# Optimization experiments

Hardware: AMD Instinct MI355X
Metric: run time of the kernel (lower is better)

## Reference

```python
import jax, jax.numpy as jnp
import numpy as np

B, S, D, H, DH, SD = 4, 512, 768, 12, 64, 30
ALPHA, BETA = 1.0, 1.0


def setup_inputs() -> dict:
    root = jax.random.key(0)
    ks = jax.random.split(root, 16)
    n = lambda k, sh: jax.random.normal(k, sh, dtype=jnp.float32)
    w = lambda k, sh: 0.02 * jax.random.normal(k, sh, dtype=jnp.float32)
    return {
        "key": n(ks[0], (B, S, D)),
        "value": n(ks[1], (B, S, D)),
        "query": n(ks[2], (B, S, D)),
        "structure": n(ks[3], (B, S, S, SD)),
        "mask": jax.random.randint(ks[4], (B, S, S), 0, 2).astype(bool),
        "Wq": w(ks[5], (D, D)), "bq": jnp.zeros((D,), jnp.float32),
        "Wk": w(ks[6], (D, D)), "bk": jnp.zeros((D,), jnp.float32),
        "Wv": w(ks[7], (D, D)), "bv": jnp.zeros((D,), jnp.float32),
        "Wsk": w(ks[8], (SD, DH)), "bsk": jnp.zeros((DH,), jnp.float32),
        "Wsv": w(ks[9], (SD, DH)), "bsv": jnp.zeros((DH,), jnp.float32),
        "Wo": w(ks[10], (D, D)), "bo": jnp.zeros((D,), jnp.float32),
    }


def reference(key, value, query, structure, mask,
              Wq, bq, Wk, bk, Wv, bv, Wsk, bsk, Wsv, bsv, Wo, bo):
    # shape: [B,S,D] -> [B,H,S,DH]
    def proj(x, W, b):
        return (x @ W + b).reshape(B, -1, H, DH).transpose(0, 2, 1, 3)

    q = proj(query, Wq, bq) / np.float32(np.sqrt(DH))  # scale applied before both score terms
    k = proj(key, Wk, bk)
    v = proj(value, Wv, bv)

    sk = structure @ Wsk + bsk  # [B,Q,K,DH] relative-structure keys
    sv = structure @ Wsv + bsv  # [B,Q,K,DH] relative-structure values

    scores = jnp.einsum('bhqd,bhkd->bhqk', q, k)
    scores = scores + ALPHA * jnp.einsum('bhqd,bqkd->bhqk', q, sk)
    scores = jnp.where(mask[:, None, :, :], jnp.float32(-1e18), scores)

    attn = jax.nn.softmax(scores, axis=-1)  # dropout p=0 -> identity

    ctx = jnp.einsum('bhqk,bhkd->bhqd', attn, v)
    ctx = ctx + BETA * jnp.einsum('bhqk,bqkd->bhqd', attn, sv)
    ctx = ctx.transpose(0, 2, 1, 3).reshape(B, S, D)

    output = ctx @ Wo + bo
    top_attn = attn[:, 0]  # [B,Q,K]
    return output, top_attn
```

## Files before the change

### kernel.cpp

```cpp
#include <hip/hip_runtime.h>
#include <hip/hip_bf16.h>

typedef unsigned int uint32_ty;

typedef float  nfloat2 __attribute__((ext_vector_type(2)));
typedef float  nfloat4 __attribute__((ext_vector_type(4)));
typedef int    nint4   __attribute__((ext_vector_type(4)));
typedef short  bf16x8  __attribute__((ext_vector_type(8)));
typedef float  f32x4   __attribute__((ext_vector_type(4)));
typedef unsigned short ushort4n __attribute__((ext_vector_type(4)));

#define BB 4
#define SS 512
#define DD 768
#define HH 12
#define DHH 64
#define SDD 30

#define LP 520

__device__ __forceinline__ float bfu(unsigned short u) {
    return __uint_as_float(((uint32_ty)u) << 16);
}
__device__ __forceinline__ unsigned short tobf(float f) {
    return __bfloat16_as_ushort(__float2bfloat16(f));
}
__device__ __forceinline__ uint32_ty pk2(float a, float b) {
    return ((uint32_ty)tobf(a)) | ((uint32_ty)tobf(b) << 16);
}
__device__ __forceinline__ void unp8(uint4 u, float* t) {
    t[0] = __uint_as_float(u.x << 16);
    t[1] = __uint_as_float(u.x & 0xFFFF0000u);
    t[2] = __uint_as_float(u.y << 16);
    t[3] = __uint_as_float(u.y & 0xFFFF0000u);
    t[4] = __uint_as_float(u.z << 16);
    t[5] = __uint_as_float(u.z & 0xFFFF0000u);
    t[6] = __uint_as_float(u.w << 16);
    t[7] = __uint_as_float(u.w & 0xFFFF0000u);
}
__device__ __forceinline__ void unp4(uint2 u, float* t) {
    t[0] = __uint_as_float(u.x << 16);
    t[1] = __uint_as_float(u.x & 0xFFFF0000u);
    t[2] = __uint_as_float(u.y << 16);
    t[3] = __uint_as_float(u.y & 0xFFFF0000u);
}

__global__ __launch_bounds__(256) void cvt_x(
    const float* __restrict__ k_in, const float* __restrict__ v_in,
    unsigned short* __restrict__ kb, unsigned short* __restrict__ vb)
{
    const float* in = blockIdx.z ? v_in : k_in;
    unsigned short* out = blockIdx.z ? vb : kb;
    size_t i = (size_t)blockIdx.x * 256 + threadIdx.x;
    const float4* p = (const float4*)in;
    float4 a = p[2 * i], b = p[2 * i + 1];
    uint4 pk;
    pk.x = pk2(a.x, a.y); pk.y = pk2(a.z, a.w);
    pk.z = pk2(b.x, b.y); pk.w = pk2(b.z, b.w);
    ((uint4*)out)[i] = pk;
}

__global__ __launch_bounds__(256) void cvt_wT(
    const float* __restrict__ W0, const float* __restrict__ W1,
    const float* __restrict__ W2, const float* __restrict__ W3,
    unsigned short* __restrict__ T0, unsigned short* __restrict__ T1,
    unsigned short* __restrict__ T2, unsigned short* __restrict__ T3)
{
    __shared__ float tile[64][65];
    int z = blockIdx.z;
    const float* W = (z == 0) ? W0 : (z == 1) ? W1 : (z == 2) ? W2 : W3;
    unsigned short* T = (z == 0) ? T0 : (z == 1) ? T1 : (z == 2) ? T2 : T3;
    int k0 = blockIdx.y * 64, n0 = blockIdx.x * 64;
    int tid = threadIdx.x;
#pragma unroll
    for (int rep = 0; rep < 4; rep++) {
        int i = tid + 256 * rep;
        int r = i >> 4, c4 = i & 15;
        float4 wv = *(const float4*)(W + (size_t)(k0 + r) * DD + n0 + 4 * c4);
        tile[r][4 * c4 + 0] = wv.x; tile[r][4 * c4 + 1] = wv.y;
        tile[r][4 * c4 + 2] = wv.z; tile[r][4 * c4 + 3] = wv.w;
    }
    __syncthreads();
#pragma unroll
    for (int rep = 0; rep < 2; rep++) {
        int i = tid + 256 * rep;
        int n = i >> 3, kc = i & 7;
        uint4 pk;
        pk.x = pk2(tile[8 * kc + 0][n], tile[8 * kc + 1][n]);
        pk.y = pk2(tile[8 * kc + 2][n], tile[8 * kc + 3][n]);
        pk.z = pk2(tile[8 * kc + 4][n], tile[8 * kc + 5][n]);
        pk.w = pk2(tile[8 * kc + 6][n], tile[8 * kc + 7][n]);
        *(uint4*)(T + (size_t)(n0 + n) * DD + k0 + 8 * kc) = pk;
    }
}

#define MBM 64
#define MBN 64
#define MBK 64
#define LDK 72

__global__ __launch_bounds__(256) void gemm_proj3(
    const float* __restrict__ Xq,
    const unsigned short* __restrict__ Xkb, const unsigned short* __restrict__ Xvb,
    const unsigned short* __restrict__ WTq, const unsigned short* __restrict__ WTk,
    const unsigned short* __restrict__ WTv,
    const float* __restrict__ bq, const float* __restrict__ bk, const float* __restrict__ bv,
    float* __restrict__ oq, unsigned short* __restrict__ okT, unsigned short* __restrict__ ov)
{
    __shared__ unsigned short As[MBM][LDK];
    __shared__ unsigned short Bs[MBN][LDK];
    int z = blockIdx.z;
    const unsigned short* WT = (z == 0) ? WTq : (z == 1) ? WTk : WTv;
    const float* bias = (z == 0) ? bq : (z == 1) ? bk : bv;

    int tid = threadIdx.x;
    int lane = tid & 63, wave = tid >> 6;
    int m0 = blockIdx.y * MBM, n0 = blockIdx.x * MBN;
    int wm = (wave >> 1) * 32, wn = (wave & 1) * 32;
    int fr = lane & 15, fq = lane >> 4;

    f32x4 acc[2][2];
#pragma unroll
    for (int i = 0; i < 2; i++)
#pragma unroll
        for (int j = 0; j < 2; j++) acc[i][j] = (f32x4){0.f, 0.f, 0.f, 0.f};

    for (int k0 = 0; k0 < DD; k0 += MBK) {
        if (z == 0) {
#pragma unroll
            for (int rep = 0; rep < 4; rep++) {
                int i = tid + 256 * rep;
                int r = i >> 4, c4 = i & 15;
                float4 xv = *(const float4*)(Xq + (size_t)(m0 + r) * DD + k0 + 4 * c4);
                ushort4n pk = {tobf(xv.x), tobf(xv.y), tobf(xv.z), tobf(xv.w)};
                *(ushort4n*)&As[r][4 * c4] = pk;
            }
        } else {
            const unsigned short* Xb = (z == 1) ? Xkb : Xvb;
#pragma unroll
            for (int rep = 0; rep < 2; rep++) {
                int i = tid + 256 * rep;
                int r = i >> 3, c = i & 7;
                *(uint4*)&As[r][8 * c] =
                    *(const uint4*)(Xb + (size_t)(m0 + r) * DD + k0 + 8 * c);
            }
        }
#pragma unroll
        for (int rep = 0; rep < 2; rep++) {
            int i = tid + 256 * rep;
            int r = i >> 3, c = i & 7;
            *(uint4*)&Bs[r][8 * c] =
                *(const uint4*)(WT + (size_t)(n0 + r) * DD + k0 + 8 * c);
        }
        __syncthreads();
#pragma unroll
        for (int ks = 0; ks < 2; ks++) {
            bf16x8 a0 = *(bf16x8*)&As[wm + fr][ks * 32 + fq * 8];
            bf16x8 a1 = *(bf16x8*)&As[wm + 16 + fr][ks * 32 + fq * 8];
            bf16x8 b0 = *(bf16x8*)&Bs[wn + fr][ks * 32 + fq * 8];
            bf16x8 b1 = *(bf16x8*)&Bs[wn + 16 + fr][ks * 32 + fq * 8];
            acc[0][0] = __builtin_amdgcn_mfma_f32_16x16x32_bf16(a0, b0, acc[0][0], 0, 0, 0);
            acc[0][1] = __builtin_amdgcn_mfma_f32_16x16x32_bf16(a0, b1, acc[0][1], 0, 0, 0);
            acc[1][0] = __builtin_amdgcn_mfma_f32_16x16x32_bf16(a1, b0, acc[1][0], 0, 0, 0);
            acc[1][1] = __builtin_amdgcn_mfma_f32_16x16x32_bf16(a1, b1, acc[1][1], 0, 0, 0);
        }
        __syncthreads();
    }

#pragma unroll
    for (int i = 0; i < 2; i++) {
#pragma unroll
        for (int j = 0; j < 2; j++) {
            int n = n0 + wn + 16 * j + fr;
            int h = n >> 6, d = n & 63;
            float bn = bias[n];
            int mbase = m0 + wm + 16 * i + fq * 4;
            int b = mbase >> 9, sbase = mbase & 511;
            if (z == 1) {
                ushort4n pk;
#pragma unroll
                for (int r = 0; r < 4; r++) pk[r] = tobf(acc[i][j][r] + bn);
                *(ushort4n*)(okT + ((((size_t)b * HH + h) * DHH + d) * SS + sbase)) = pk;
            } else if (z == 0) {
#pragma unroll
                for (int r = 0; r < 4; r++)
                    oq[((((size_t)b * HH + h) * SS + sbase + r) * DHH + d)] =
                        (acc[i][j][r] + bn) * 0.125f;
            } else {
#pragma unroll
                for (int r = 0; r < 4; r++)
                    ov[((((size_t)b * HH + h) * SS + sbase + r) * DHH + d)] =
                        tobf(acc[i][j][r] + bn);
            }
        }
    }
}

__global__ __launch_bounds__(256) void gemm_out(
    const unsigned short* __restrict__ ctxb, const unsigned short* __restrict__ WoT,
    const float* __restrict__ bias, float* __restrict__ out)
{
    __shared__ unsigned short As[MBM][LDK];
    __shared__ unsigned short Bs[MBN][LDK];
    int tid = threadIdx.x;
    int lane = tid & 63, wave = tid >> 6;
    int m0 = blockIdx.y * MBM, n0 = blockIdx.x * MBN;
    int wm = (wave >> 1) * 32, wn = (wave & 1) * 32;
    int fr = lane & 15, fq = lane >> 4;

    f32x4 acc[2][2];
#pragma unroll
    for (int i = 0; i < 2; i++)
#pragma unroll
        for (int j = 0; j < 2; j++) acc[i][j] = (f32x4){0.f, 0.f, 0.f, 0.f};

    for (int k0 = 0; k0 < DD; k0 += MBK) {
#pragma unroll
        for (int rep = 0; rep < 2; rep++) {
            int i = tid + 256 * rep;
            int r = i >> 3, c = i & 7;
            *(uint4*)&As[r][8 * c] =
                *(const uint4*)(ctxb + (size_t)(m0 + r) * DD + k0 + 8 * c);
        }
#pragma unroll
        for (int rep = 0; rep < 2; rep++) {
            int i = tid + 256 * rep;
            int r = i >> 3, c = i & 7;
            *(uint4*)&Bs[r][8 * c] =
                *(const uint4*)(WoT + (size_t)(n0 + r) * DD + k0 + 8 * c);
        }
        __syncthreads();
#pragma unroll
        for (int ks = 0; ks < 2; ks++) {
            bf16x8 a0 = *(bf16x8*)&As[wm + fr][ks * 32 + fq * 8];
            bf16x8 a1 = *(bf16x8*)&As[wm + 16 + fr][ks * 32 + fq * 8];
            bf16x8 b0 = *(bf16x8*)&Bs[wn + fr][ks * 32 + fq * 8];
            bf16x8 b1 = *(bf16x8*)&Bs[wn + 16 + fr][ks * 32 + fq * 8];
            acc[0][0] = __builtin_amdgcn_mfma_f32_16x16x32_bf16(a0, b0, acc[0][0], 0, 0, 0);
            acc[0][1] = __builtin_amdgcn_mfma_f32_16x16x32_bf16(a0, b1, acc[0][1], 0, 0, 0);
            acc[1][0] = __builtin_amdgcn_mfma_f32_16x16x32_bf16(a1, b0, acc[1][0], 0, 0, 0);
            acc[1][1] = __builtin_amdgcn_mfma_f32_16x16x32_bf16(a1, b1, acc[1][1], 0, 0, 0);
        }
        __syncthreads();
    }

#pragma unroll
    for (int i = 0; i < 2; i++) {
#pragma unroll
        for (int j = 0; j < 2; j++) {
            int n = n0 + wn + 16 * j + fr;
            float bn = bias[n];
            int mbase = m0 + wm + 16 * i + fq * 4;
#pragma unroll
            for (int r = 0; r < 4; r++)
                out[(size_t)(mbase + r) * DD + n] = acc[i][j][r] + bn;
        }
    }
}

__global__ __launch_bounds__(256) void attn_fused(
    const float* __restrict__ q,
    const unsigned short* __restrict__ kT,
    const unsigned short* __restrict__ v,
    const float* __restrict__ structure,
    const int* __restrict__ mask,
    const float* __restrict__ Wsk,
    const float* __restrict__ bsk,
    const float* __restrict__ Wsv,
    const float* __restrict__ bsv,
    unsigned short* __restrict__ ctxb,
    float* __restrict__ top_attn)
{
    __shared__ float qs[HH][DHH];
    __shared__ unsigned short stT[SDD][LP];
    __shared__ float qt_s[HH][SDD];
    __shared__ float qb_s[HH];
    __shared__ float astr_s[HH][SDD];
    __shared__ unsigned short at[HH][LP];

    int tid = threadIdx.x;
    int lane = tid & 63, wave = tid >> 6;

    int blk = blockIdx.x;
    int xcd = blk & 7;
    int b = xcd >> 1;
    int qp = ((xcd & 1) << 8) | (blk >> 3);

    for (int i = tid; i < HH * DHH; i += 256) {
        int h = i >> 6, d = i & 63;
        qs[h][d] = q[(((size_t)b * HH + h) * SS + qp) * DHH + d];
    }
    {
        const float* srow = structure + ((size_t)b * SS + qp) * (size_t)(SS * SDD);
        for (int k = tid; k < SS; k += 256) {
            const nfloat2* rp = (const nfloat2*)(srow + (size_t)k * SDD);
#pragma unroll
            for (int w = 0; w < 15; w++) {
                nfloat2 xv = __builtin_nontemporal_load(rp + w);
                stT[2 * w][k] = tobf(xv.x);
                stT[2 * w + 1][k] = tobf(xv.y);
            }
        }
    }
    __syncthreads();

    for (int i = tid; i < HH * SDD; i += 256) {
        int h = i / SDD, si = i % SDD;
        const float4* wp = (const float4*)(Wsk + si * DHH);
        const float4* qp4 = (const float4*)qs[h];
        float a = 0.f;
#pragma unroll
        for (int d4 = 0; d4 < 16; d4++) {
            float4 wv = wp[d4];
            float4 qv = qp4[d4];
            a += qv.x * wv.x + qv.y * wv.y + qv.z * wv.z + qv.w * wv.w;
        }
        qt_s[h][si] = a;
    }
    if (tid < HH) {
        const float4* bp = (const float4*)bsk;
        const float4* qp4 = (const float4*)qs[tid];
        float a = 0.f;
#pragma unroll
        for (int d4 = 0; d4 < 16; d4++) {
            float4 wv = bp[d4];
            float4 qv = qp4[d4];
            a += qv.x * wv.x + qv.y * wv.y + qv.z * wv.z + qv.w * wv.w;
        }
        qb_s[tid] = a;
    }
    __syncthreads();

    int h0 = wave * 3;
    float attnv[3][8];
#pragma unroll
    for (int h = 0; h < 3; h++)
#pragma unroll
        for (int j = 0; j < 8; j++) attnv[h][j] = 0.f;

#pragma unroll 2
    for (int si = 0; si < SDD; si++) {
        uint4 sv4 = *(const uint4*)&stT[si][8 * lane];
        float t[8];
        unp8(sv4, t);
#pragma unroll
        for (int h = 0; h < 3; h++) {
            float qt = qt_s[h0 + h][si];
#pragma unroll
            for (int j = 0; j < 8; j++) attnv[h][j] += qt * t[j];
        }
    }

    {
        const unsigned short* kbase = kT + (((size_t)b * HH + h0) * DHH) * SS + 8 * lane;
#pragma unroll
        for (int h = 0; h < 3; h++) {
            const unsigned short* kp = kbase + (size_t)h * (DHH * SS);
            float acc[8] = {0.f, 0.f, 0.f, 0.f, 0.f, 0.f, 0.f, 0.f};
#pragma unroll 8
            for (int d = 0; d < DHH; d++) {
                float qd = qs[h0 + h][d];
                uint4 kv = *(const uint4*)(kp + (size_t)d * SS);
                float t[8];
                unp8(kv, t);
#pragma unroll
                for (int j = 0; j < 8; j++) acc[j] += qd * t[j];
            }
            float qb = qb_s[h0 + h];
#pragma unroll
            for (int j = 0; j < 8; j++) attnv[h][j] += acc[j] + qb;
        }
    }

    {
        const int* mrow = mask + ((size_t)b * SS + qp) * SS + 8 * lane;
        nint4 m0v = __builtin_nontemporal_load((const nint4*)mrow);
        nint4 m1v = __builtin_nontemporal_load(((const nint4*)mrow) + 1);
        int mm[8] = {m0v.x, m0v.y, m0v.z, m0v.w, m1v.x, m1v.y, m1v.z, m1v.w};
#pragma unroll
        for (int h = 0; h < 3; h++)
#pragma unroll
            for (int j = 0; j < 8; j++)
                if (mm[j]) attnv[h][j] = -1e18f;
    }

#pragma unroll
    for (int h = 0; h < 3; h++) {
        float m = attnv[h][0];
#pragma unroll
        for (int j = 1; j < 8; j++) m = fmaxf(m, attnv[h][j]);
#pragma unroll
        for (int off = 32; off > 0; off >>= 1) m = fmaxf(m, __shfl_xor(m, off));
        float l = 0.f;
#pragma unroll
        for (int j = 0; j < 8; j++) { attnv[h][j] = __expf(attnv[h][j] - m); l += attnv[h][j]; }
#pragma unroll
        for (int off = 32; off > 0; off >>= 1) l += __shfl_xor(l, off);
        float inv = 1.f / l;
        float a[8];
#pragma unroll
        for (int j = 0; j < 8; j++) a[j] = attnv[h][j] * inv;
        uint4 pk;
        pk.x = (uint32_ty)tobf(a[0]) | ((uint32_ty)tobf(a[1]) << 16);
        pk.y = (uint32_ty)tobf(a[2]) | ((uint32_ty)tobf(a[3]) << 16);
        pk.z = (uint32_ty)tobf(a[4]) | ((uint32_ty)tobf(a[5]) << 16);
        pk.w = (uint32_ty)tobf(a[6]) | ((uint32_ty)tobf(a[7]) << 16);
        *(uint4*)&at[h0 + h][8 * lane] = pk;
        if (h0 + h == 0) {
            float* tp = top_attn + ((size_t)b * SS + qp) * SS + 8 * lane;
            nfloat4 w0 = {a[0], a[1], a[2], a[3]};
            nfloat4 w1 = {a[4], a[5], a[6], a[7]};
            __builtin_nontemporal_store(w0, (nfloat4*)tp);
            __builtin_nontemporal_store(w1, ((nfloat4*)tp) + 1);
        }
    }
    __syncthreads();

    if (tid < 180) {
        int h = tid / 15, sp = tid % 15;
        int si0 = 2 * sp, si1 = si0 + 1;
        float a0e = 0.f, a0o = 0.f, a1e = 0.f, a1o = 0.f;
#pragma unroll 2
        for (int j = 0; j < 64; j++) {
            uint4 av = *(const uint4*)&at[h][8 * j];
            uint4 s0 = *(const uint4*)&stT[si0][8 * j];
            uint4 s1 = *(const uint4*)&stT[si1][8 * j];
            float a[8], t0[8], t1[8];
            unp8(av, a); unp8(s0, t0); unp8(s1, t1);
#pragma unroll
            for (int t = 0; t < 8; t += 2) {
                a0e += a[t] * t0[t];     a0o += a[t + 1] * t0[t + 1];
                a1e += a[t] * t1[t];     a1o += a[t + 1] * t1[t + 1];
            }
        }
        astr_s[h][si0] = a0e + a0o;
        astr_s[h][si1] = a1e + a1o;
    }
    __syncthreads();

    if (tid < 192) {
        int h = tid >> 4, dq = tid & 15;
        const unsigned short* vp = v + ((size_t)b * HH + h) * (size_t)(SS * DHH) + 4 * dq;
        float4 ae; ae.x = ae.y = ae.z = ae.w = 0.f;
        float4 ao; ao.x = ao.y = ao.z = ao.w = 0.f;
#pragma unroll 2
        for (int j = 0; j < 64; j++) {
            uint4 av = *(const uint4*)&at[h][8 * j];
            float a[8];
            unp8(av, a);
            const unsigned short* vk = vp + (size_t)(8 * j) * DHH;
#pragma unroll
            for (int t = 0; t < 8; t += 2) {
                uint2 v0 = *(const uint2*)(vk + (size_t)t * DHH);
                uint2 v1 = *(const uint2*)(vk + (size_t)(t + 1) * DHH);
                float f0[4], f1[4];
                unp4(v0, f0); unp4(v1, f1);
                ae.x += a[t] * f0[0]; ae.y += a[t] * f0[1];
                ae.z += a[t] * f0[2]; ae.w += a[t] * f0[3];
                ao.x += a[t + 1] * f1[0]; ao.y += a[t + 1] * f1[1];
                ao.z += a[t + 1] * f1[2]; ao.w += a[t + 1] * f1[3];
            }
        }
        float4 sa = *(const float4*)(bsv + 4 * dq);
#pragma unroll
        for (int si = 0; si < SDD; si++) {
            float as = astr_s[h][si];
            float4 wv = *(const float4*)(Wsv + si * DHH + 4 * dq);
            sa.x += as * wv.x; sa.y += as * wv.y;
            sa.z += as * wv.z; sa.w += as * wv.w;
        }
        ushort4n co;
        co[0] = tobf(ae.x + ao.x + sa.x);
        co[1] = tobf(ae.y + ao.y + sa.y);
        co[2] = tobf(ae.z + ao.z + sa.z);
        co[3] = tobf(ae.w + ao.w + sa.w);
        *(ushort4n*)(ctxb + ((size_t)b * SS + qp) * DD + h * DHH + 4 * dq) = co;
    }
}

extern "C" void kernel_launch(void* const* d_in, const int* in_sizes, int n_in,
                              void* d_out, int out_size, void* d_ws, size_t ws_size,
                              hipStream_t stream)
{
    const float* key       = (const float*)d_in[0];
    const float* value     = (const float*)d_in[1];
    const float* query     = (const float*)d_in[2];
    const float* structure = (const float*)d_in[3];
    const int*   mask      = (const int*)d_in[4];
    const float* Wq  = (const float*)d_in[5];
    const float* bq  = (const float*)d_in[6];
    const float* Wk  = (const float*)d_in[7];
    const float* bk  = (const float*)d_in[8];
    const float* Wv  = (const float*)d_in[9];
    const float* bv  = (const float*)d_in[10];
    const float* Wsk = (const float*)d_in[11];
    const float* bsk = (const float*)d_in[12];
    const float* Wsv = (const float*)d_in[13];
    const float* bsv = (const float*)d_in[14];
    const float* Wo  = (const float*)d_in[15];
    const float* bo  = (const float*)d_in[16];

    float* out_main = (float*)d_out;
    float* out_attn = (float*)d_out + (size_t)BB * SS * DD;

    unsigned short* u = (unsigned short*)d_ws;
    unsigned short* Xb_k  = u;
    unsigned short* Xb_v  = u + 1572864;
    unsigned short* WT_q  = u + 3145728;
    unsigned short* WT_k  = u + 3735552;
    unsigned short* WT_v  = u + 4325376;
    unsigned short* WT_o  = u + 4915200;
    unsigned short* kT_b  = u + 5505024;
    unsigned short* v_b   = u + 7077888;
    float*          q_buf = (float*)(u + 8650752);
    unsigned short* ctx_b = Xb_k;

    cvt_x<<<dim3(768, 1, 2), dim3(256), 0, stream>>>(key, value, Xb_k, Xb_v);
    cvt_wT<<<dim3(12, 12, 4), dim3(256), 0, stream>>>(Wq, Wk, Wv, Wo,
                                                      WT_q, WT_k, WT_v, WT_o);

    dim3 ggrd3(DD / MBN, (BB * SS) / MBM, 3);
    gemm_proj3<<<ggrd3, dim3(256), 0, stream>>>(query, Xb_k, Xb_v,
                                                WT_q, WT_k, WT_v,
                                                bq, bk, bv, q_buf, kT_b, v_b);

    attn_fused<<<BB * SS, 256, 0, stream>>>(q_buf, kT_b, v_b, structure, mask,
                                            Wsk, bsk, Wsv, bsv, ctx_b, out_attn);

    dim3 ggrd(DD / MBN, (BB * SS) / MBM);
    gemm_out<<<ggrd, dim3(256), 0, stream>>>(ctx_b, WT_o, bo, out_main);
}
```

Before: 476.5 us.

## Split P·V reduction across all threads and merge conversion kernels into one launch

The attention kernel's attn·V accumulation was previously done by only 192 of 256 threads over all 512 keys. It now splits the key range into four chunks handled by all threads, writes partial sums into the reused structure shared buffer, and reduces them after a barrier. The two input/weight conversion kernels are also merged into a single prepack launch to save one launch. The trade-off is an extra barrier and shared-memory round trip, plus many idle blocks in the merged launch grid.

```diff
diff --git a/kernel.cpp b/kernel.cpp
--- a/kernel.cpp
+++ b/kernel.cpp
@@ -45,33 +45,34 @@
     t[3] = __uint_as_float(u.y & 0xFFFF0000u);
 }
 
-__global__ __launch_bounds__(256) void cvt_x(
-    const float* __restrict__ k_in, const float* __restrict__ v_in,
-    unsigned short* __restrict__ kb, unsigned short* __restrict__ vb)
-{
-    const float* in = blockIdx.z ? v_in : k_in;
-    unsigned short* out = blockIdx.z ? vb : kb;
-    size_t i = (size_t)blockIdx.x * 256 + threadIdx.x;
-    const float4* p = (const float4*)in;
-    float4 a = p[2 * i], b = p[2 * i + 1];
-    uint4 pk;
-    pk.x = pk2(a.x, a.y); pk.y = pk2(a.z, a.w);
-    pk.z = pk2(b.x, b.y); pk.w = pk2(b.z, b.w);
-    ((uint4*)out)[i] = pk;
-}
-
-__global__ __launch_bounds__(256) void cvt_wT(
+__global__ __launch_bounds__(256) void prepack(
+    const float* __restrict__ key, const float* __restrict__ value,
     const float* __restrict__ W0, const float* __restrict__ W1,
     const float* __restrict__ W2, const float* __restrict__ W3,
+    unsigned short* __restrict__ kb, unsigned short* __restrict__ vb,
     unsigned short* __restrict__ T0, unsigned short* __restrict__ T1,
     unsigned short* __restrict__ T2, unsigned short* __restrict__ T3)
 {
     __shared__ float tile[64][65];
     int z = blockIdx.z;
-    const float* W = (z == 0) ? W0 : (z == 1) ? W1 : (z == 2) ? W2 : W3;
-    unsigned short* T = (z == 0) ? T0 : (z == 1) ? T1 : (z == 2) ? T2 : T3;
-    int k0 = blockIdx.y * 64, n0 = blockIdx.x * 64;
     int tid = threadIdx.x;
+    if (z < 2) {
+        const float* in = z ? value : key;
+        unsigned short* out = z ? vb : kb;
+        size_t i = (size_t)blockIdx.x * 256 + tid;
+        const float4* p = (const float4*)in;
+        float4 a = p[2 * i], b = p[2 * i + 1];
+        uint4 pk;
+        pk.x = pk2(a.x, a.y); pk.y = pk2(a.z, a.w);
+        pk.z = pk2(b.x, b.y); pk.w = pk2(b.z, b.w);
+        ((uint4*)out)[i] = pk;
+        return;
+    }
+    if (blockIdx.x >= 144) return;
+    int zz = z - 2;
+    const float* W = (zz == 0) ? W0 : (zz == 1) ? W1 : (zz == 2) ? W2 : W3;
+    unsigned short* T = (zz == 0) ? T0 : (zz == 1) ? T1 : (zz == 2) ? T2 : T3;
+    int k0 = (blockIdx.x / 12) * 64, n0 = (blockIdx.x % 12) * 64;
 #pragma unroll
     for (int rep = 0; rep < 4; rep++) {
         int i = tid + 256 * rep;
@@ -272,7 +273,7 @@
     float* __restrict__ top_attn)
 {
     __shared__ float qs[HH][DHH];
-    __shared__ unsigned short stT[SDD][LP];
+    __shared__ __align__(16) unsigned short stT[SDD][LP];
     __shared__ float qt_s[HH][SDD];
     __shared__ float qb_s[HH];
     __shared__ float astr_s[HH][SDD];
@@ -438,13 +439,18 @@
     }
     __syncthreads();
 
-    if (tid < 192) {
-        int h = tid >> 4, dq = tid & 15;
+    float4* pvp = (float4*)&stT[0][0];
+#pragma unroll
+    for (int r = 0; r < 3; r++) {
+        int job = tid + 256 * r;
+        int kq = job / 192;
+        int rem = job - kq * 192;
+        int h = rem >> 4, dq = rem & 15;
         const unsigned short* vp = v + ((size_t)b * HH + h) * (size_t)(SS * DHH) + 4 * dq;
         float4 ae; ae.x = ae.y = ae.z = ae.w = 0.f;
         float4 ao; ao.x = ao.y = ao.z = ao.w = 0.f;
 #pragma unroll 2
-        for (int j = 0; j < 64; j++) {
+        for (int j = 16 * kq; j < 16 * kq + 16; j++) {
             uint4 av = *(const uint4*)&at[h][8 * j];
             float a[8];
             unp8(av, a);
@@ -461,6 +467,21 @@
                 ao.z += a[t + 1] * f1[2]; ao.w += a[t + 1] * f1[3];
             }
         }
+        float4 ps;
+        ps.x = ae.x + ao.x; ps.y = ae.y + ao.y;
+        ps.z = ae.z + ao.z; ps.w = ae.w + ao.w;
+        pvp[job] = ps;
+    }
+    __syncthreads();
+
+    if (tid < 192) {
+        int h = tid >> 4, dq = tid & 15;
+        float4 s = pvp[tid];
+#pragma unroll
+        for (int kq = 1; kq < 4; kq++) {
+            float4 p = pvp[kq * 192 + tid];
+            s.x += p.x; s.y += p.y; s.z += p.z; s.w += p.w;
+        }
         float4 sa = *(const float4*)(bsv + 4 * dq);
 #pragma unroll
         for (int si = 0; si < SDD; si++) {
@@ -470,10 +491,10 @@
             sa.z += as * wv.z; sa.w += as * wv.w;
         }
         ushort4n co;
-        co[0] = tobf(ae.x + ao.x + sa.x);
-        co[1] = tobf(ae.y + ao.y + sa.y);
-        co[2] = tobf(ae.z + ao.z + sa.z);
-        co[3] = tobf(ae.w + ao.w + sa.w);
+        co[0] = tobf(s.x + sa.x);
+        co[1] = tobf(s.y + sa.y);
+        co[2] = tobf(s.z + sa.z);
+        co[3] = tobf(s.w + sa.w);
         *(ushort4n*)(ctxb + ((size_t)b * SS + qp) * DD + h * DHH + 4 * dq) = co;
     }
 }
@@ -515,9 +536,8 @@
     float*          q_buf = (float*)(u + 8650752);
     unsigned short* ctx_b = Xb_k;
 
-    cvt_x<<<dim3(768, 1, 2), dim3(256), 0, stream>>>(key, value, Xb_k, Xb_v);
-    cvt_wT<<<dim3(12, 12, 4), dim3(256), 0, stream>>>(Wq, Wk, Wv, Wo,
-                                                      WT_q, WT_k, WT_v, WT_o);
+    prepack<<<dim3(768, 1, 6), dim3(256), 0, stream>>>(
+        key, value, Wq, Wk, Wv, Wo, Xb_k, Xb_v, WT_q, WT_k, WT_v, WT_o);
 
     dim3 ggrd3(DD / MBN, (BB * SS) / MBM, 3);
     gemm_proj3<<<ggrd3, dim3(256), 0, stream>>>(query, Xb_k, Xb_v,
```

New measurement: 479.5 us. No clear change (+0.6%).
